# Optimization experiments

Measured on AMD Instinct MI355X. Metric: run time of the kernel, lower is better.

## Reference

```python
import jax, jax.numpy as jnp
import numpy as np

DIM = 128; NH = 4; WS = 7; SS = 3
ZP, HP, WP = 14, 56, 56
NMLP = 512; EPS = 1e-5
N = WS ** 3  # tokens per window (343)


def _ln(x, g, b):
    m = x.mean(-1, keepdims=True)
    v = x.var(-1, keepdims=True)
    return (x - m) / jnp.sqrt(v + EPS) * g + b


def _rel_index():
    # static relative-position index for a cubic (WS,WS,WS) window
    c = np.stack(np.meshgrid(np.arange(WS), np.arange(WS), np.arange(WS), indexing='ij')).reshape(3, -1)
    rel = (c[:, :, None] - c[:, None, :]).transpose(1, 2, 0) + (WS - 1)
    rel[..., 0] *= (2 * WS - 1) ** 2
    rel[..., 1] *= (2 * WS - 1)
    return rel.sum(-1).reshape(-1)  # [N*N]


def _attn_mask():
    # static shifted-window attention mask, [nW, N, N]
    img = np.zeros((ZP, HP, WP), np.float32)
    cnt = 0
    sl = (slice(0, -WS), slice(-WS, -SS), slice(-SS, None))
    for z in sl:
        for h in sl:
            for w in sl:
                img[z, h, w] = cnt
                cnt += 1
    m = img.reshape(ZP // WS, WS, HP // WS, WS, WP // WS, WS)
    m = m.transpose(0, 2, 4, 1, 3, 5).reshape(-1, N)
    d = m[:, None, :] - m[:, :, None]
    return np.where(d != 0, np.float32(-100.0), np.float32(0.0))


_REL_IDX = jnp.asarray(_rel_index())
_MASK = jnp.asarray(_attn_mask())


def setup_inputs() -> dict:
    key = jax.random.key(0)
    ks = jax.random.split(key, 8)
    return {
        'x': jax.random.normal(ks[0], (2, ZP, HP, WP, DIM), jnp.float32),
        'norm1_g': jnp.ones((DIM,), jnp.float32),
        'norm1_b': jnp.zeros((DIM,), jnp.float32),
        'qkv_w': jax.random.normal(ks[1], (DIM, 3 * DIM), jnp.float32) * 0.02,
        'qkv_b': jnp.zeros((3 * DIM,), jnp.float32),
        'rel_table': jax.random.normal(ks[2], ((2 * WS - 1) ** 3, NH), jnp.float32) * 0.02,
        'proj_w': jax.random.normal(ks[3], (DIM, DIM), jnp.float32) * 0.02,
        'proj_b': jnp.zeros((DIM,), jnp.float32),
        'norm2_g': jnp.ones((DIM,), jnp.float32),
        'norm2_b': jnp.zeros((DIM,), jnp.float32),
        'fc1_w': jax.random.normal(ks[4], (DIM, NMLP), jnp.float32) * 0.02,
        'fc1_b': jnp.zeros((NMLP,), jnp.float32),
        'fc2_w': jax.random.normal(ks[5], (NMLP, DIM), jnp.float32) * 0.02,
        'fc2_b': jnp.zeros((DIM,), jnp.float32),
    }


def reference(x, norm1_g, norm1_b, qkv_w, qkv_b, rel_table, proj_w, proj_b,
              norm2_g, norm2_b, fc1_w, fc1_b, fc2_w, fc2_b):
    B, Z, H, W, C = x.shape
    hd = C // NH
    scale = hd ** -0.5
    shortcut = x
    xn = _ln(x, norm1_g, norm1_b)
    # cyclic shift
    xs = jnp.roll(xn, (-SS, -SS, -SS), axis=(1, 2, 3))
    # window partition -> [B*nW, N, C]
    xw = xs.reshape(B, Z // WS, WS, H // WS, WS, W // WS, WS, C)
    xw = xw.transpose(0, 1, 3, 5, 2, 4, 6, 7).reshape(-1, N, C)
    qkv = (xw @ qkv_w + qkv_b).reshape(-1, N, 3, NH, hd).transpose(2, 0, 3, 1, 4)
    q, k, v = qkv[0], qkv[1], qkv[2]  # [Bn, NH, N, hd]
    attn = jnp.einsum('bhnd,bhmd->bhnm', q * scale, k)
    bias = rel_table[_REL_IDX].reshape(N, N, NH).transpose(2, 0, 1)  # [NH, N, N]
    attn = attn + bias[None]
    nW = _MASK.shape[0]
    attn = attn.reshape(B, nW, NH, N, N) + _MASK[None, :, None]
    attn = jax.nn.softmax(attn.reshape(-1, NH, N, N), axis=-1)
    out = jnp.einsum('bhnm,bhmd->bhnd', attn, v)
    out = out.transpose(0, 2, 1, 3).reshape(-1, N, C)
    out = out @ proj_w + proj_b
    # window reverse -> [B, Z, H, W, C]
    out = out.reshape(B, Z // WS, H // WS, W // WS, WS, WS, WS, C)
    out = out.transpose(0, 1, 4, 2, 5, 3, 6, 7).reshape(B, Z, H, W, C)
    out = jnp.roll(out, (SS, SS, SS), axis=(1, 2, 3))
    x1 = shortcut + out
    y = _ln(x1, norm2_g, norm2_b)
    y = jax.nn.gelu(y @ fc1_w + fc1_b, approximate=False) @ fc2_w + fc2_b
    return x1 + y
```

## Files before the change

kernel.cpp:

```cpp
#include <hip/hip_runtime.h>


typedef __attribute__((ext_vector_type(8))) _Float16 half8;
typedef __attribute__((ext_vector_type(4))) _Float16 half4;
typedef __attribute__((ext_vector_type(4))) float floatx4;

#define DEV static __device__ __forceinline__

DEV floatx4 MFMA(half8 a, half8 b, floatx4 c) {
  return __builtin_amdgcn_mfma_f32_16x16x32_f16(a, b, c, 0, 0, 0);
}
DEV floatx4 MFMA16(half4 a, half4 b, floatx4 c) {
  return __builtin_amdgcn_mfma_f32_16x16x16f16(a, b, c, 0, 0, 0);
}

DEV float gelu_f(float v) {
  return v / (1.f + __expf(-1.702f * v));
}

DEV void f4arr(float4 v, float o[4]) {
  o[0] = v.x; o[1] = v.y; o[2] = v.z; o[3] = v.w;
}

DEV void stage_load(half8 pf[8], const _Float16* src, int rst, int tid) {
#pragma unroll
  for (int it = 0; it < 8; ++it) {
    int e = it * 256 + tid;
    int row = e >> 4, seg = e & 15;
    pf[it] = *(const half8*)&src[(size_t)row * rst + seg * 8];
  }
}
DEV void stage_store(_Float16* wb, const half8 pf[8], int tid) {
#pragma unroll
  for (int it = 0; it < 8; ++it) {
    int e = it * 256 + tid;
    int row = e >> 4, seg = e & 15;
    *(half8*)&wb[row * 136 + seg * 8] = pf[it];
  }
}
DEV void stage_tile(_Float16* wb, const _Float16* src, int rst, int tid) {
  half8 pf[8];
  stage_load(pf, src, rst, tid);
  stage_store(wb, pf, tid);
}

__global__ __launch_bounds__(256) void k_prep(
    const float* __restrict__ rel, _Float16* __restrict__ biasH,
    const float* __restrict__ w1, const float* __restrict__ w2,
    const float* __restrict__ wq, const float* __restrict__ wp,
    _Float16* __restrict__ w1h, _Float16* __restrict__ w2h,
    _Float16* __restrict__ wqh, _Float16* __restrict__ wph) {
  int gid = blockIdx.x * 256 + threadIdx.x;
  if (gid < 495616) {
    int reg = gid & 3, quad = (gid >> 2) & 3, ml = (gid >> 4) & 15;
    int t = gid >> 8;
    int rt = t % 22; t /= 22;
    int nt = t % 22; int h = t / 22;
    int q = rt * 16 + ml, kv = nt * 16 + quad * 4 + reg;
    float val = -30000.f;
    if (q < 343 && kv < 343) {
      int lzi = q / 49, ri = q - lzi * 49, lhi = ri / 7, lwi = ri - lhi * 7;
      int lzj = kv / 49, rj = kv - lzj * 49, lhj = rj / 7, lwj = rj - lhj * 7;
      int idx = (lzi - lzj + 6) * 169 + (lhi - lhj + 6) * 13 + (lwi - lwj + 6);
      val = rel[idx * 4 + h];
    }
    biasH[gid] = (_Float16)val;
    return;
  }
  int i = gid - 495616;
  if (i < 65536) {
    int n = i >> 7, k = i & 127;
    w1h[i] = (_Float16)w1[k * 512 + n];
  } else if (i < 131072) {
    int j = i - 65536; int n = j >> 9, k = j & 511;
    w2h[j] = (_Float16)w2[k * 128 + n];
  } else if (i < 180224) {
    int j = i - 131072; int n = j >> 7, k = j & 127;
    wqh[j] = (_Float16)wq[k * 384 + n];
  } else if (i < 196608) {
    int j = i - 180224; int n = j >> 7, k = j & 127;
    wph[j] = (_Float16)wp[k * 128 + n];
  }
}

__global__ __launch_bounds__(256) void k_ln_qkv(
    const float* __restrict__ x, const float* __restrict__ g1,
    const float* __restrict__ b1, const _Float16* __restrict__ wqh,
    const float* __restrict__ bq, _Float16* __restrict__ qkv) {
  __shared__ __align__(16) _Float16 wb[128 * 136];
  const int tid = threadIdx.x, lane = tid & 63, wid = tid >> 6;
  const int ml = lane & 15, quad = lane >> 4;
  const int task = blockIdx.x * 4 + wid;
  const int w = task / 11, pr = task - (task / 11) * 11;
  const int b_ = w >> 7, r = w & 127;
  const int wz = r >> 6, wh = (r >> 3) & 7, ww = r & 7;

  half8 a0[4], a1[4];
#pragma unroll
  for (int hf = 0; hf < 2; ++hf) {
    int t = pr * 32 + hf * 16 + ml; if (t > 342) t = 342;
    int lz = t / 49, rr = t - lz * 49, lh = rr / 7, lw = rr - lh * 7;
    int oz = wz * 7 + lz + 3; if (oz >= 14) oz -= 14;
    int oh = wh * 7 + lh + 3; if (oh >= 56) oh -= 56;
    int ow = ww * 7 + lw + 3; if (ow >= 56) ow -= 56;
    const float* xp = x + ((((b_ * 14 + oz) * 56 + oh) * 56 + ow) << 7);
    float xv[32];
    float s = 0.f, ss = 0.f;
#pragma unroll
    for (int ks = 0; ks < 4; ++ks) {
      float4 p0 = *(const float4*)(xp + ks * 32 + quad * 8);
      float4 p1 = *(const float4*)(xp + ks * 32 + quad * 8 + 4);
      xv[ks * 8 + 0] = p0.x; xv[ks * 8 + 1] = p0.y; xv[ks * 8 + 2] = p0.z; xv[ks * 8 + 3] = p0.w;
      xv[ks * 8 + 4] = p1.x; xv[ks * 8 + 5] = p1.y; xv[ks * 8 + 6] = p1.z; xv[ks * 8 + 7] = p1.w;
      s += (p0.x + p0.y) + (p0.z + p0.w) + (p1.x + p1.y) + (p1.z + p1.w);
      ss += (p0.x * p0.x + p0.y * p0.y) + (p0.z * p0.z + p0.w * p0.w) +
            (p1.x * p1.x + p1.y * p1.y) + (p1.z * p1.z + p1.w * p1.w);
    }
    s += __shfl_xor(s, 16); s += __shfl_xor(s, 32);
    ss += __shfl_xor(ss, 16); ss += __shfl_xor(ss, 32);
    float mean = s * 0.0078125f;
    float rstd = rsqrtf(ss * 0.0078125f - mean * mean + 1e-5f);
#pragma unroll
    for (int ks = 0; ks < 4; ++ks) {
      int k0 = ks * 32 + quad * 8;
      float4 gg0 = *(const float4*)(g1 + k0), gg1 = *(const float4*)(g1 + k0 + 4);
      float4 bb0 = *(const float4*)(b1 + k0), bb1 = *(const float4*)(b1 + k0 + 4);
      half8 a;
      a[0] = (_Float16)((xv[ks * 8 + 0] - mean) * rstd * gg0.x + bb0.x);
      a[1] = (_Float16)((xv[ks * 8 + 1] - mean) * rstd * gg0.y + bb0.y);
      a[2] = (_Float16)((xv[ks * 8 + 2] - mean) * rstd * gg0.z + bb0.z);
      a[3] = (_Float16)((xv[ks * 8 + 3] - mean) * rstd * gg0.w + bb0.w);
      a[4] = (_Float16)((xv[ks * 8 + 4] - mean) * rstd * gg1.x + bb1.x);
      a[5] = (_Float16)((xv[ks * 8 + 5] - mean) * rstd * gg1.y + bb1.y);
      a[6] = (_Float16)((xv[ks * 8 + 6] - mean) * rstd * gg1.z + bb1.z);
      a[7] = (_Float16)((xv[ks * 8 + 7] - mean) * rstd * gg1.w + bb1.w);
      if (hf == 0) a0[ks] = a; else a1[ks] = a;
    }
  }

  const int t0 = pr * 32 + ml;
  const int t1 = t0 + 16;
  _Float16* q0 = qkv + ((size_t)w * 343 + t0) * 384;
  _Float16* q1 = qkv + ((size_t)w * 343 + (t1 < 343 ? t1 : 342)) * 384;

  for (int c = 0; c < 3; ++c) {
    __syncthreads();
    stage_tile(wb, wqh + (size_t)c * 128 * 128, 128, tid);
    __syncthreads();
    for (int ntl = 0; ntl < 8; ++ntl) {
      floatx4 acc0 = {0.f, 0.f, 0.f, 0.f}, acc1 = {0.f, 0.f, 0.f, 0.f};
#pragma unroll
      for (int ks = 0; ks < 4; ++ks) {
        half8 bb = *(const half8*)&wb[(ntl * 16 + ml) * 136 + ks * 32 + quad * 8];
        acc0 = MFMA(bb, a0[ks], acc0);
        acc1 = MFMA(bb, a1[ks], acc1);
      }
      const int colb = c * 128 + ntl * 16 + quad * 4;
      float qb[4]; f4arr(*(const float4*)&bq[colb], qb);
      half4 s0, s1;
#pragma unroll
      for (int reg = 0; reg < 4; ++reg) {
        s0[reg] = (_Float16)(acc0[reg] + qb[reg]);
        s1[reg] = (_Float16)(acc1[reg] + qb[reg]);
      }
      *(half4*)&q0[colb] = s0;
      if (t1 < 343) *(half4*)&q1[colb] = s1;
    }
  }
}

__global__ __launch_bounds__(512, 2) void k_attn(const _Float16* __restrict__ qkv,
                                                 const _Float16* __restrict__ biasH,
                                                 _Float16* __restrict__ aout) {
  __shared__ __align__(16) _Float16 kl[352 * 40];
  __shared__ __align__(16) _Float16 vt[32 * 364];
  __shared__ __align__(4) unsigned char region[352];
  const int tid = threadIdx.x;
  const int w = blockIdx.x >> 2, head = blockIdx.x & 3;
  const int r = w & 127;
  const int wz = r >> 6, wh = (r >> 3) & 7, ww = r & 7;
  const bool fz = (wz == 1), fh = (wh == 7), fw = (ww == 7);

  for (int t = tid; t < 352; t += 512) {
    int rg = 255;
    if (t < 343) {
      int lz = t / 49, rr = t - lz * 49, lh = rr / 7, lw = rr - lh * 7;
      int rz = fz ? (lz < 4 ? 1 : 2) : 0;
      int rh2 = fh ? (lh < 4 ? 1 : 2) : 0;
      int rw2 = fw ? (lw < 4 ? 1 : 2) : 0;
      rg = rz * 9 + rh2 * 3 + rw2;
    }
    region[t] = (unsigned char)rg;
  }
  const _Float16* qkvw = qkv + (size_t)w * 343 * 384;
  for (int e = tid; e < 352 * 4; e += 512) {
    int t = e >> 2, d8 = (e & 3) * 8;
    half8 v;
    if (t < 343) {
      v = *(const half8*)&qkvw[t * 384 + 128 + head * 32 + d8];
    } else {
#pragma unroll
      for (int j = 0; j < 8; ++j) v[j] = (_Float16)0.f;
    }
    *(half8*)&kl[t * 40 + d8] = v;
  }
  for (int e = tid; e < 343 * 4; e += 512) {
    int t = e >> 2, d8 = (e & 3) * 8;
    half8 v = *(const half8*)&qkvw[t * 384 + 256 + head * 32 + d8];
#pragma unroll
    for (int j = 0; j < 8; ++j) vt[(d8 + j) * 364 + t] = v[j];
  }
  for (int e = tid; e < 9 * 32; e += 512) {
    int t = 343 + (e >> 5), d = e & 31;
    vt[d * 364 + t] = (_Float16)0.f;
  }
  __syncthreads();

  const int lane = tid & 63, wid = tid >> 6;
  const int ml = lane & 15, quad = lane >> 4;
  const float scale = 0.17677669529663687f;

  for (int rt = wid; rt < 22; rt += 8) {
    const int row0 = rt * 16;
    int qrow = row0 + ml; if (qrow > 342) qrow = 342;
    half8 bq8 = *(const half8*)&qkvw[qrow * 384 + head * 32 + quad * 8];
    const int rq = region[qrow];
    const int bbase = (head * 484 + rt) * 256 + ml * 16 + quad * 4;

    floatx4 o0 = {0.f, 0.f, 0.f, 0.f}, o1 = {0.f, 0.f, 0.f, 0.f};
    floatx4 sm4 = {0.f, 0.f, 0.f, 0.f};
#pragma unroll
    for (int nt = 0; nt < 22; ++nt) {
      half8 ak = *(const half8*)&kl[(nt * 16 + ml) * 40 + quad * 8];
      floatx4 S = MFMA(ak, bq8, (floatx4){0.f, 0.f, 0.f, 0.f});
      half4 b4 = *(const half4*)&biasH[bbase + nt * 5632];
      uchar4 rc = *(const uchar4*)&region[nt * 16 + quad * 4];
      const unsigned char* rcp = (const unsigned char*)&rc;
      half4 p;
#pragma unroll
      for (int reg = 0; reg < 4; ++reg) {
        float v = fmaf(S[reg], scale, (float)b4[reg]);
        if (rcp[reg] != rq) v = -30000.f;
        float e = __expf(v);
        sm4[reg] += e;
        p[reg] = (_Float16)e;
      }
      half4 va0 = *(const half4*)&vt[ml * 364 + nt * 16 + quad * 4];
      half4 va1 = *(const half4*)&vt[(16 + ml) * 364 + nt * 16 + quad * 4];
      o0 = MFMA16(va0, p, o0);
      o1 = MFMA16(va1, p, o1);
    }
    float sm = (sm4[0] + sm4[1]) + (sm4[2] + sm4[3]);
    sm += __shfl_xor(sm, 16);
    sm += __shfl_xor(sm, 32);

    const int orow = row0 + ml;
    if (orow < 343) {
      float inv = 1.f / sm;
      _Float16* op = aout + ((size_t)w * 343 + orow) * 128 + head * 32;
      half4 s0, s1;
#pragma unroll
      for (int reg = 0; reg < 4; ++reg) {
        s0[reg] = (_Float16)(o0[reg] * inv);
        s1[reg] = (_Float16)(o1[reg] * inv);
      }
      *(half4*)&op[quad * 4] = s0;
      *(half4*)&op[16 + quad * 4] = s1;
    }
  }
}

__global__ __launch_bounds__(256, 2) void k_pm(
    const _Float16* __restrict__ aout, const _Float16* __restrict__ wph,
    const float* __restrict__ bp, const float* __restrict__ x,
    const float* __restrict__ g2, const float* __restrict__ nb2,
    const _Float16* __restrict__ w1h, const float* __restrict__ bfc1,
    const _Float16* __restrict__ w2h, const float* __restrict__ bfc2,
    float* __restrict__ out) {
  __shared__ __align__(16) _Float16 hc[4][32 * 136];
  __shared__ __align__(16) _Float16 wb[128 * 136];
  const int tid = threadIdx.x, lane = tid & 63, wid = tid >> 6;
  const int ml = lane & 15, quad = lane >> 4;
  const int task = blockIdx.x * 4 + wid;
  const int w = task / 11, pr = task - (task / 11) * 11;
  const int b_ = w >> 7, r = w & 127;
  const int wz = r >> 6, wh = (r >> 3) & 7, ww = r & 7;
  const _Float16* ap = aout + (size_t)w * 343 * 128;
  _Float16* hw = &hc[wid][0];

  half8 pf[8];
  stage_load(pf, wph, 128, tid);

  int ra = pr * 32 + ml; if (ra > 342) ra = 342;
  int rbm = pr * 32 + 16 + ml; if (rbm > 342) rbm = 342;
  half8 a0[4], a1[4];
#pragma unroll
  for (int ks = 0; ks < 4; ++ks) {
    a0[ks] = *(const half8*)&ap[ra * 128 + ks * 32 + quad * 8];
    a1[ks] = *(const half8*)&ap[rbm * 128 + ks * 32 + quad * 8];
  }
  int tok[2];
#pragma unroll
  for (int mt = 0; mt < 2; ++mt) {
    int t = pr * 32 + mt * 16 + ml;
    if (t < 343) {
      int lz = t / 49, rr = t - lz * 49, lh = rr / 7, lw = rr - lh * 7;
      int oz = wz * 7 + lz + 3; if (oz >= 14) oz -= 14;
      int oh = wh * 7 + lh + 3; if (oh >= 56) oh -= 56;
      int ow = ww * 7 + lw + 3; if (ow >= 56) ow -= 56;
      tok[mt] = ((b_ * 14 + oz) * 56 + oh) * 56 + ow;
    } else {
      tok[mt] = -1;
    }
  }
  stage_store(wb, pf, tid);
  __syncthreads();
  stage_load(pf, w1h, 128, tid);

  floatx4 px[8][2];
  for (int nt = 0; nt < 8; ++nt) {
    floatx4 acc0 = {0.f, 0.f, 0.f, 0.f}, acc1 = {0.f, 0.f, 0.f, 0.f};
#pragma unroll
    for (int ks = 0; ks < 4; ++ks) {
      half8 bb = *(const half8*)&wb[(nt * 16 + ml) * 136 + ks * 32 + quad * 8];
      acc0 = MFMA(bb, a0[ks], acc0);
      acc1 = MFMA(bb, a1[ks], acc1);
    }
    const int colb = nt * 16 + quad * 4;
    float pb4[4]; f4arr(*(const float4*)&bp[colb], pb4);
    float xr0[4] = {0.f, 0.f, 0.f, 0.f}, xr1[4] = {0.f, 0.f, 0.f, 0.f};
    if (tok[0] >= 0) f4arr(*(const float4*)&x[(size_t)tok[0] * 128 + colb], xr0);
    if (tok[1] >= 0) f4arr(*(const float4*)&x[(size_t)tok[1] * 128 + colb], xr1);
#pragma unroll
    for (int reg = 0; reg < 4; ++reg) {
      px[nt][0][reg] = acc0[reg] + pb4[reg] + xr0[reg];
      px[nt][1][reg] = acc1[reg] + pb4[reg] + xr1[reg];
    }
  }

  float mean[2], rstd[2];
#pragma unroll
  for (int mt = 0; mt < 2; ++mt) {
    float s = 0.f, ss = 0.f;
#pragma unroll
    for (int nt = 0; nt < 8; ++nt)
#pragma unroll
      for (int reg = 0; reg < 4; ++reg) {
        float v = px[nt][mt][reg];
        s += v; ss += v * v;
      }
    s += __shfl_xor(s, 16); s += __shfl_xor(s, 32);
    ss += __shfl_xor(ss, 16); ss += __shfl_xor(ss, 32);
    float m = s * 0.0078125f;
    mean[mt] = m;
    rstd[mt] = rsqrtf(ss * 0.0078125f - m * m + 1e-5f);
  }

  for (int nt = 0; nt < 8; ++nt) {
    const int colb = nt * 16 + quad * 4;
    float g4[4], nb4[4];
    f4arr(*(const float4*)&g2[colb], g4);
    f4arr(*(const float4*)&nb2[colb], nb4);
#pragma unroll
    for (int mt = 0; mt < 2; ++mt) {
      half4 h;
#pragma unroll
      for (int reg = 0; reg < 4; ++reg)
        h[reg] = (_Float16)((px[nt][mt][reg] - mean[mt]) * rstd[mt] * g4[reg] + nb4[reg]);
      *(half4*)&hw[(mt * 16 + ml) * 136 + colb] = h;
    }
  }
  half8 ay[2][4];
#pragma unroll
  for (int mt = 0; mt < 2; ++mt)
#pragma unroll
    for (int ks = 0; ks < 4; ++ks)
      ay[mt][ks] = *(const half8*)&hw[(mt * 16 + ml) * 136 + ks * 32 + quad * 8];

  floatx4 acc2[8][2];
#pragma unroll
  for (int nt = 0; nt < 8; ++nt)
#pragma unroll
    for (int mt = 0; mt < 2; ++mt) acc2[nt][mt] = (floatx4){0.f, 0.f, 0.f, 0.f};

  for (int ch = 0; ch < 4; ++ch) {
    __syncthreads();
    stage_store(wb, pf, tid);
    __syncthreads();
    stage_load(pf, w2h + (size_t)ch * 128, 512, tid);
    for (int nt = 0; nt < 8; ++nt) {
      floatx4 f0 = {0.f, 0.f, 0.f, 0.f}, f1 = {0.f, 0.f, 0.f, 0.f};
#pragma unroll
      for (int ks = 0; ks < 4; ++ks) {
        half8 bb = *(const half8*)&wb[(nt * 16 + ml) * 136 + ks * 32 + quad * 8];
        f0 = MFMA(bb, ay[0][ks], f0);
        f1 = MFMA(bb, ay[1][ks], f1);
      }
      const int colb = nt * 16 + quad * 4;
      float fb4[4]; f4arr(*(const float4*)&bfc1[ch * 128 + colb], fb4);
      half4 h0, h1;
#pragma unroll
      for (int reg = 0; reg < 4; ++reg) {
        h0[reg] = (_Float16)gelu_f(f0[reg] + fb4[reg]);
        h1[reg] = (_Float16)gelu_f(f1[reg] + fb4[reg]);
      }
      *(half4*)&hw[ml * 136 + colb] = h0;
      *(half4*)&hw[(16 + ml) * 136 + colb] = h1;
    }
    __syncthreads();
    stage_store(wb, pf, tid);
    __syncthreads();
    if (ch < 3) stage_load(pf, w1h + (size_t)(ch + 1) * 128 * 128, 128, tid);
#pragma unroll
    for (int ks = 0; ks < 4; ++ks) {
      half8 A0 = *(const half8*)&hw[ml * 136 + ks * 32 + quad * 8];
      half8 A1 = *(const half8*)&hw[(16 + ml) * 136 + ks * 32 + quad * 8];
#pragma unroll
      for (int nt = 0; nt < 8; ++nt) {
        half8 bb = *(const half8*)&wb[(nt * 16 + ml) * 136 + ks * 32 + quad * 8];
        acc2[nt][0] = MFMA(bb, A0, acc2[nt][0]);
        acc2[nt][1] = MFMA(bb, A1, acc2[nt][1]);
      }
    }
  }

  for (int nt = 0; nt < 8; ++nt) {
    const int colb = nt * 16 + quad * 4;
    float fb4[4]; f4arr(*(const float4*)&bfc2[colb], fb4);
#pragma unroll
    for (int mt = 0; mt < 2; ++mt) {
      if (tok[mt] >= 0) {
        float4 o;
        o.x = px[nt][mt][0] + acc2[nt][mt][0] + fb4[0];
        o.y = px[nt][mt][1] + acc2[nt][mt][1] + fb4[1];
        o.z = px[nt][mt][2] + acc2[nt][mt][2] + fb4[2];
        o.w = px[nt][mt][3] + acc2[nt][mt][3] + fb4[3];
        *(float4*)&out[(size_t)tok[mt] * 128 + colb] = o;
      }
    }
  }
}

extern "C" void kernel_launch(void* const* d_in, const int* in_sizes, int n_in,
                              void* d_out, int out_size, void* d_ws, size_t ws_size,
                              hipStream_t stream) {
  (void)in_sizes; (void)n_in; (void)out_size; (void)ws_size;
  const float* x   = (const float*)d_in[0];
  const float* g1  = (const float*)d_in[1];
  const float* b1  = (const float*)d_in[2];
  const float* wq  = (const float*)d_in[3];
  const float* bq  = (const float*)d_in[4];
  const float* rel = (const float*)d_in[5];
  const float* wp  = (const float*)d_in[6];
  const float* bp  = (const float*)d_in[7];
  const float* g2  = (const float*)d_in[8];
  const float* b2_ = (const float*)d_in[9];
  const float* w1  = (const float*)d_in[10];
  const float* bf1 = (const float*)d_in[11];
  const float* w2  = (const float*)d_in[12];
  const float* bf2 = (const float*)d_in[13];

  char* ws = (char*)d_ws;
  _Float16* qkv   = (_Float16*)(ws);
  _Float16* aout  = (_Float16*)(ws + 67436544);
  _Float16* biasH = (_Float16*)(ws + 89915392);
  _Float16* w1h   = (_Float16*)(ws + 91897856);
  _Float16* w2h   = (_Float16*)(ws + 92028928);
  _Float16* wqh   = (_Float16*)(ws + 92160000);
  _Float16* wph   = (_Float16*)(ws + 92258304);
  float*    out   = (float*)d_out;

  hipLaunchKernelGGL(k_prep,   dim3(2704), dim3(256), 0, stream,
                     rel, biasH, w1, w2, wq, wp, w1h, w2h, wqh, wph);
  hipLaunchKernelGGL(k_ln_qkv, dim3(704),  dim3(256), 0, stream, x, g1, b1, wqh, bq, qkv);
  hipLaunchKernelGGL(k_attn,   dim3(1024), dim3(512), 0, stream, qkv, biasH, aout);
  hipLaunchKernelGGL(k_pm,     dim3(704),  dim3(256), 0, stream,
                     aout, wph, bp, x, g2, b2_, w1h, bf1, w2h, bf2, out);
}
```

Before: 329.3 us.

## Batch attention tiles, precompute region penalty table, make bias tiles contiguous

Reorders the precomputed fp16 bias so the 22 key tiles for a given query tile sit contiguously in memory. Replaces the per-element region comparison with a shared-memory penalty table, indexed by query region, that is added to the bias in half precision. Processes key tiles in groups of eight, issuing all bias loads and QK MFMAs before the exp/PV stage to hide latency. This costs about 19KB more LDS, which could reduce occupancy, plus more registers. Adding -30000 in fp16 to the bias stays finite, so masked entries are still suppressed.

Result: faster. 281.5 us, median of 3 (-14.5%).

```diff
diff --git a/kernel.cpp b/kernel.cpp
--- a/kernel.cpp
+++ b/kernel.cpp
@@ -53,9 +53,9 @@
   int gid = blockIdx.x * 256 + threadIdx.x;
   if (gid < 495616) {
     int reg = gid & 3, quad = (gid >> 2) & 3, ml = (gid >> 4) & 15;
-    int t = gid >> 8;
-    int rt = t % 22; t /= 22;
-    int nt = t % 22; int h = t / 22;
+    int u = gid >> 8;
+    int nt = u % 22; u /= 22;
+    int rt = u % 22; int h = u / 22;
     int q = rt * 16 + ml, kv = nt * 16 + quad * 4 + reg;
     float val = -30000.f;
     if (q < 343 && kv < 343) {
@@ -174,6 +174,7 @@
                                                  _Float16* __restrict__ aout) {
   __shared__ __align__(16) _Float16 kl[352 * 40];
   __shared__ __align__(16) _Float16 vt[32 * 364];
+  __shared__ __align__(16) _Float16 pen[27 * 360];
   __shared__ __align__(4) unsigned char region[352];
   const int tid = threadIdx.x;
   const int w = blockIdx.x >> 2, head = blockIdx.x & 3;
@@ -192,6 +193,18 @@
     }
     region[t] = (unsigned char)rg;
   }
+  for (int e = tid; e < 27 * 352; e += 512) {
+    int rg = e / 352, t = e - rg * 352;
+    int rt_ = 255;
+    if (t < 343) {
+      int lz = t / 49, rr = t - lz * 49, lh = rr / 7, lw = rr - lh * 7;
+      int rz = fz ? (lz < 4 ? 1 : 2) : 0;
+      int rh2 = fh ? (lh < 4 ? 1 : 2) : 0;
+      int rw2 = fw ? (lw < 4 ? 1 : 2) : 0;
+      rt_ = rz * 9 + rh2 * 3 + rw2;
+    }
+    pen[rg * 360 + t] = (rt_ == rg) ? (_Float16)0.f : (_Float16)(-30000.f);
+  }
   const _Float16* qkvw = qkv + (size_t)w * 343 * 384;
   for (int e = tid; e < 352 * 4; e += 512) {
     int t = e >> 2, d8 = (e & 3) * 8;
@@ -225,30 +238,43 @@
     int qrow = row0 + ml; if (qrow > 342) qrow = 342;
     half8 bq8 = *(const half8*)&qkvw[qrow * 384 + head * 32 + quad * 8];
     const int rq = region[qrow];
-    const int bbase = (head * 484 + rt) * 256 + ml * 16 + quad * 4;
+    const _Float16* penr = &pen[rq * 360 + quad * 4];
+    const _Float16* bb = &biasH[(size_t)((head * 22 + rt) * 22) * 256 + ml * 16 + quad * 4];
 
     floatx4 o0 = {0.f, 0.f, 0.f, 0.f}, o1 = {0.f, 0.f, 0.f, 0.f};
     floatx4 sm4 = {0.f, 0.f, 0.f, 0.f};
 #pragma unroll
-    for (int nt = 0; nt < 22; ++nt) {
-      half8 ak = *(const half8*)&kl[(nt * 16 + ml) * 40 + quad * 8];
-      floatx4 S = MFMA(ak, bq8, (floatx4){0.f, 0.f, 0.f, 0.f});
-      half4 b4 = *(const half4*)&biasH[bbase + nt * 5632];
-      uchar4 rc = *(const uchar4*)&region[nt * 16 + quad * 4];
-      const unsigned char* rcp = (const unsigned char*)&rc;
-      half4 p;
-#pragma unroll
-      for (int reg = 0; reg < 4; ++reg) {
-        float v = fmaf(S[reg], scale, (float)b4[reg]);
-        if (rcp[reg] != rq) v = -30000.f;
-        float e = __expf(v);
-        sm4[reg] += e;
-        p[reg] = (_Float16)e;
-      }
-      half4 va0 = *(const half4*)&vt[ml * 364 + nt * 16 + quad * 4];
-      half4 va1 = *(const half4*)&vt[(16 + ml) * 364 + nt * 16 + quad * 4];
-      o0 = MFMA16(va0, p, o0);
-      o1 = MFMA16(va1, p, o1);
+    for (int g = 0; g < 3; ++g) {
+      const int G = (g < 2) ? 8 : 6;
+      const int nb = g * 8;
+      half4 bp[8];
+      floatx4 S[8];
+#pragma unroll
+      for (int k = 0; k < 8; ++k) if (k < G) {
+        half4 b4 = *(const half4*)&bb[(nb + k) * 256];
+        half4 p4 = *(const half4*)&penr[(nb + k) * 16];
+        bp[k] = b4 + p4;
+      }
+#pragma unroll
+      for (int k = 0; k < 8; ++k) if (k < G) {
+        half8 ak = *(const half8*)&kl[((nb + k) * 16 + ml) * 40 + quad * 8];
+        S[k] = MFMA(ak, bq8, (floatx4){0.f, 0.f, 0.f, 0.f});
+      }
+#pragma unroll
+      for (int k = 0; k < 8; ++k) if (k < G) {
+        half4 p;
+#pragma unroll
+        for (int reg = 0; reg < 4; ++reg) {
+          float v = fmaf(S[k][reg], scale, (float)bp[k][reg]);
+          float e = __expf(v);
+          sm4[reg] += e;
+          p[reg] = (_Float16)e;
+        }
+        half4 va0 = *(const half4*)&vt[ml * 364 + (nb + k) * 16 + quad * 4];
+        half4 va1 = *(const half4*)&vt[(16 + ml) * 364 + (nb + k) * 16 + quad * 4];
+        o0 = MFMA16(va0, p, o0);
+        o1 = MFMA16(va1, p, o1);
+      }
     }
     float sm = (sm4[0] + sm4[1]) + (sm4[2] + sm4[3]);
     sm += __shfl_xor(sm, 16);
```
